# Optimization experiments

Measured on AMD Instinct MI355X. Metric: run time of the kernel, lower is better.

Reference implementation:

```python
import jax, jax.numpy as jnp
import numpy as np

H = 16  # num_heads
LN_EPS = 1e-5


def setup_inputs() -> dict:
    key = jax.random.key(0)
    ks = jax.random.split(key, 9)
    B, T, D = 2, 2048, 1024
    s = D ** -0.5
    return {
        "q": jax.random.normal(ks[0], (B, T, D), jnp.float32),
        "k": jax.random.normal(ks[1], (B, T, D), jnp.float32),
        "v": jax.random.normal(ks[2], (B, T, D), jnp.float32),
        "wq": jax.random.normal(ks[3], (D, D), jnp.float32) * s,
        "bq": jnp.zeros((D,), jnp.float32),
        "wk": jax.random.normal(ks[4], (D, D), jnp.float32) * s,
        "bk": jnp.zeros((D,), jnp.float32),
        "wv": jax.random.normal(ks[5], (D, D), jnp.float32) * s,
        "bv": jnp.zeros((D,), jnp.float32),
        "ln_g": jnp.ones((D,), jnp.float32),
        "ln_b": jnp.zeros((D,), jnp.float32),
    }


def _layernorm(x, g, b):
    mu = jnp.mean(x, axis=-1, keepdims=True)
    var = jnp.mean(jnp.square(x - mu), axis=-1, keepdims=True)
    return (x - mu) * jax.lax.rsqrt(var + LN_EPS) * g + b


def reference(q, k, v, wq, bq, wk, bk, wv, bv, ln_g, ln_b):
    B, T, D = q.shape
    dh = D // H
    residual = q
    qp = q @ wq.T + bq
    kp = k @ wk.T + bk
    vp = v @ wv.T + bv
    # faithful to torch: flat row-major view (B,T,D) -> (H*B, T, dh)
    qh = qp.reshape(H * B, T, dh)
    kh = kp.reshape(H * B, T, dh)
    vh = vp.reshape(H * B, T, dh)
    scores = jnp.einsum('btd,bsd->bts', qh, kh) * (dh ** -0.5)  # (H*B, T, T)
    attn = jax.nn.softmax(scores, axis=-1)
    ctx = jnp.einsum('bts,bsd->btd', attn, vh)  # (H*B, T, dh)
    ctx = ctx.reshape(B, T, D)
    out = _layernorm(residual + ctx, ln_g, ln_b)
    return (out, attn)
```

## Files before the change

kernel.cpp:

```cpp
#include <hip/hip_runtime.h>

typedef unsigned short u16;
typedef __attribute__((ext_vector_type(8))) short s8v;
typedef __attribute__((ext_vector_type(4))) float f4v;

#define MFMA16(a, b, c) __builtin_amdgcn_mfma_f32_16x16x32_bf16(a, b, c, 0, 0, 0)

#define TSEQ 2048
#define NTOK 4096
#define HEADS 32
#define HB_ELEMS 131072

__device__ __forceinline__ unsigned cvt_pk(float lo, float hi) {
  unsigned r;
  asm("v_cvt_pk_bf16_f32 %0, %1, %2" : "=v"(r) : "v"(lo), "v"(hi));
  return r;
}

__device__ __forceinline__ void gl_lds16(const u16* g, u16* l) {
  __builtin_amdgcn_global_load_lds(
      (const __attribute__((address_space(1))) void*)g,
      (__attribute__((address_space(3))) void*)l, 16, 0, 0);
}

__global__ void cvt_all(const float* __restrict__ q, const float* __restrict__ k,
                        const float* __restrict__ v, const float* __restrict__ wq,
                        const float* __restrict__ wk, const float* __restrict__ wv,
                        u16* __restrict__ dst) {
  int i = (blockIdx.x * blockDim.x + threadIdx.x) * 4;
  const float* src; int off;
  if (i < 12582912) {
    int s = i >> 22; src = (s == 0) ? q : ((s == 1) ? k : v); off = i & 4194303;
  } else {
    int j = i - 12582912;
    int s = j >> 20; src = (s == 0) ? wq : ((s == 1) ? wk : wv); off = j & 1048575;
  }
  float4 val = *(const float4*)(src + off);
  uint2 o;
  o.x = cvt_pk(val.x, val.y);
  o.y = cvt_pk(val.z, val.w);
  *(uint2*)(dst + i) = o;
}

__launch_bounds__(256, 3)
__global__ void proj_gemm(const u16* __restrict__ Aall, const u16* __restrict__ Wall,
                          const float* __restrict__ bqp, const float* __restrict__ bkp,
                          const float* __restrict__ bvp, u16* __restrict__ Call) {
  const int z = blockIdx.z;
  const u16* A = Aall + (size_t)z * 4194304;
  const u16* W = Wall + (size_t)z * 1048576;
  u16* C = Call + (size_t)z * 4194304;
  const float* bias = (z == 0) ? bqp : ((z == 1) ? bkp : bvp);

  __shared__ __align__(16) u16 SH[17408];
  u16* As = SH;
  u16* Bs = SH + 8192;

  const int tid = threadIdx.x;
  const int w = tid >> 6, lane = tid & 63, g = lane >> 4, l = lane & 15;
  const int wr = w >> 1, wc = w & 1;
  const int tr = blockIdx.y * 128, tc = blockIdx.x * 128;

  const int srow = tid >> 3;
  const int scol = (tid & 7) * 8;

  f4v acc[4][4] = {};

  for (int kt = 0; kt < 1024; kt += 64) {
#pragma unroll
    for (int c4 = 0; c4 < 4; ++c4) {
      gl_lds16(A + (size_t)(tr + c4 * 32 + srow) * 1024 + kt + scol,
               As + c4 * 2048 + tid * 8);
      gl_lds16(W + (size_t)(tc + c4 * 32 + srow) * 1024 + kt + scol,
               Bs + c4 * 2048 + tid * 8);
    }
    __syncthreads();
#pragma unroll
    for (int ks = 0; ks < 2; ++ks) {
      s8v a[4], bb[4];
#pragma unroll
      for (int m = 0; m < 4; ++m)
        a[m] = *(const s8v*)(As + (wr * 64 + m * 16 + l) * 64 + ks * 32 + g * 8);
#pragma unroll
      for (int n = 0; n < 4; ++n)
        bb[n] = *(const s8v*)(Bs + (wc * 64 + n * 16 + l) * 64 + ks * 32 + g * 8);
#pragma unroll
      for (int m = 0; m < 4; ++m)
#pragma unroll
        for (int n = 0; n < 4; ++n)
          acc[m][n] = MFMA16(a[m], bb[n], acc[m][n]);
    }
    __syncthreads();
  }
  u16* T = SH;
#pragma unroll
  for (int m = 0; m < 4; ++m)
#pragma unroll
    for (int n = 0; n < 4; ++n) {
      int d = wc * 64 + n * 16 + l;
      float bv = bias[tc + d];
      unsigned c01 = cvt_pk(acc[m][n][0] + bv, acc[m][n][1] + bv);
      unsigned c23 = cvt_pk(acc[m][n][2] + bv, acc[m][n][3] + bv);
      int t0 = wr * 64 + m * 16 + g * 4;
      T[(t0 + 0) * 136 + d] = (u16)c01;
      T[(t0 + 1) * 136 + d] = (u16)(c01 >> 16);
      T[(t0 + 2) * 136 + d] = (u16)c23;
      T[(t0 + 3) * 136 + d] = (u16)(c23 >> 16);
    }
  __syncthreads();
#pragma unroll
  for (int it = 0; it < 8; ++it) {
    int t = it * 16 + (tid >> 4);
    int c8 = (tid & 15) * 8;
    *(s8v*)(C + (size_t)(tr + t) * 1024 + tc + c8) = *(const s8v*)&T[t * 136 + c8];
  }
}

__global__ void vtrans(const u16* __restrict__ vp, u16* __restrict__ vT) {
  const int hb = blockIdx.y;
  const int t0 = blockIdx.x * 64;
  const int tid = threadIdx.x;
  __shared__ u16 tl[64][65];
  const u16* vph = vp + (size_t)hb * HB_ELEMS;
  u16* vth = vT + (size_t)hb * HB_ELEMS;
#pragma unroll
  for (int it = 0; it < 4; ++it) {
    int i = (tid + it * 256) * 4;
    int r = i >> 6, c = i & 63;
    *(ushort4*)&tl[r][c] = *(const ushort4*)(vph + (size_t)(t0 + r) * 64 + c);
  }
  __syncthreads();
#pragma unroll
  for (int it = 0; it < 4; ++it) {
    int i = (tid + it * 256) * 4;
    int d = i >> 6, j = i & 63;
    ushort4 o;
    o.x = tl[j + 0][d]; o.y = tl[j + 1][d]; o.z = tl[j + 2][d]; o.w = tl[j + 3][d];
    *(ushort4*)(vth + (size_t)d * TSEQ + t0 + j) = o;
  }
}

__launch_bounds__(512, 2)
__global__ void attn_fused(const u16* __restrict__ qp, const u16* __restrict__ kp,
                           const u16* __restrict__ vT, float* __restrict__ attn,
                           float* __restrict__ ctx) {
  const int hw = blockIdx.x + (blockIdx.y << 4);
  const int hb = (hw & 7) + ((hw >> 7) << 3);
  const int qt = (hw >> 3) & 15;

  const int tid = threadIdx.x;
  const int w = tid >> 6, lane = tid & 63, g = lane >> 4, l = lane & 15;
  const int lx = l & 7;

  const u16* qh = qp + (size_t)hb * HB_ELEMS;
  const u16* kh = kp + (size_t)hb * HB_ELEMS;
  const u16* vh = vT + (size_t)hb * HB_ELEMS;

  __shared__ __align__(16) u16 SH[35840];

  const int row0 = qt * 128 + w * 16;
  const float scale = 0.125f;

  const int srow = tid >> 3;
  const int swc = ((tid & 7) ^ (srow & 7)) * 8;

  s8v qf0 = *(const s8v*)(qh + (size_t)(row0 + l) * 64 + g * 8);
  s8v qf1 = *(const s8v*)(qh + (size_t)(row0 + l) * 64 + 32 + g * 8);

#define STAGE1(buf, kt4_) do { const int c0_ = (kt4_) * 256;                    \
    _Pragma("unroll")                                                           \
    for (int c4 = 0; c4 < 4; ++c4)                                              \
      gl_lds16(kh + (size_t)(c0_ + c4 * 64 + srow) * 64 + swc,                  \
               (buf) + c4 * 4096 + tid * 8);                                    \
  } while (0)

  u16* Ka = SH;
  u16* Kb = SH + 16384;

  float sum = 0.0f;
  STAGE1(Ka, 0);
  asm volatile("s_waitcnt vmcnt(0)" ::: "memory");
  __builtin_amdgcn_sched_barrier(0);
  __builtin_amdgcn_s_barrier();
  for (int kt4 = 0; kt4 < 8; ++kt4) {
    const u16* kbuf = (kt4 & 1) ? Kb : Ka;
    if (kt4 < 7) STAGE1((kt4 & 1) ? Ka : Kb, kt4 + 1);
#pragma unroll
    for (int q4 = 0; q4 < 4; ++q4) {
#pragma unroll
      for (int n = 0; n < 4; ++n) {
        const u16* kr = kbuf + q4 * 4096 + (n * 16 + l) * 64;
        s8v b0 = *(const s8v*)(kr + (g ^ lx) * 8);
        s8v b1 = *(const s8v*)(kr + ((4 + g) ^ lx) * 8);
        f4v s = {};
        s = MFMA16(b0, qf0, s);
        s = MFMA16(b1, qf1, s);
        sum += __expf(s[0] * scale) + __expf(s[1] * scale)
             + __expf(s[2] * scale) + __expf(s[3] * scale);
      }
    }
    asm volatile("s_waitcnt lgkmcnt(0)" ::: "memory");
    asm volatile("s_waitcnt vmcnt(0)" ::: "memory");
    __builtin_amdgcn_sched_barrier(0);
    __builtin_amdgcn_s_barrier();
  }
#undef STAGE1
  sum += __shfl_xor(sum, 16);
  sum += __shfl_xor(sum, 32);
  const float inv = 1.0f / sum;

  u16* K0 = SH;
  u16* V0 = SH + 8192;
  float* Pf = (float*)(SH + 16384);

#define STAGE2(b, kt_) do { const int c0_ = (kt_) * 64;                          \
    gl_lds16(kh + (size_t)(c0_ + srow) * 64 + swc, K0 + (b) * 4096 + tid * 8);   \
    gl_lds16(vh + (size_t)srow * TSEQ + c0_ + swc, V0 + (b) * 4096 + tid * 8);   \
  } while (0)

  f4v cacc[4] = {};
  float* attn_h = attn + (size_t)hb * TSEQ * TSEQ;
  const int kt0 = (qt * 2 + ((hw >> 7) << 3)) & 31;
  const int prow = w * 16 + l;
  const int sr4 = lane >> 4;
  const int sc = (lane & 15) * 4;

  STAGE2(0, kt0);
  asm volatile("s_waitcnt vmcnt(0)" ::: "memory");
  __builtin_amdgcn_sched_barrier(0);
  __builtin_amdgcn_s_barrier();

  for (int i = 0; i < 32; ++i) {
    const int cur = i & 1;
    const int col0 = ((i + kt0) & 31) * 64;
    const u16* Kl = K0 + cur * 4096;
    const u16* Vl = V0 + cur * 4096;
    if (i < 31) STAGE2(cur ^ 1, (i + 1 + kt0) & 31);
#pragma unroll
    for (int n = 0; n < 4; ++n) {
      const u16* kr = Kl + (n * 16 + l) * 64;
      s8v b0 = *(const s8v*)(kr + (g ^ lx) * 8);
      s8v b1 = *(const s8v*)(kr + ((4 + g) ^ lx) * 8);
      f4v s = {};
      s = MFMA16(b0, qf0, s);
      s = MFMA16(b1, qf1, s);
      f4v p;
#pragma unroll
      for (int r = 0; r < 4; ++r) p[r] = __expf(s[r] * scale) * inv;
      *(f4v*)&Pf[prow * 76 + n * 16 + g * 4] = p;
    }
    asm volatile("s_waitcnt lgkmcnt(0)" ::: "memory");
    __builtin_amdgcn_sched_barrier(0);
#pragma unroll
    for (int ks = 0; ks < 2; ++ks) {
      const float* pr = &Pf[prow * 76 + ks * 32 + g * 8];
      f4v r0 = *(const f4v*)pr;
      f4v r1 = *(const f4v*)(pr + 4);
      union { unsigned u[4]; s8v s; } pc;
      pc.u[0] = cvt_pk(r0[0], r0[1]);
      pc.u[1] = cvt_pk(r0[2], r0[3]);
      pc.u[2] = cvt_pk(r1[0], r1[1]);
      pc.u[3] = cvt_pk(r1[2], r1[3]);
      s8v pa = pc.s;
#pragma unroll
      for (int n4 = 0; n4 < 4; ++n4) {
        const u16* vr = Vl + (n4 * 16 + l) * 64;
        s8v bvv = *(const s8v*)(vr + ((ks * 4 + g) ^ lx) * 8);
        cacc[n4] = MFMA16(pa, bvv, cacc[n4]);
      }
    }
#pragma unroll
    for (int r4 = 0; r4 < 4; ++r4) {
      const int row = w * 16 + r4 * 4 + sr4;
      f4v pv_ = *(const f4v*)&Pf[row * 76 + sc];
      *(f4v*)(attn_h + (size_t)(qt * 128 + row) * TSEQ + col0 + sc) = pv_;
    }
    if (i < 31) {
      asm volatile("s_waitcnt lgkmcnt(0)" ::: "memory");
      asm volatile("s_waitcnt vmcnt(4)" ::: "memory");
      __builtin_amdgcn_sched_barrier(0);
      __builtin_amdgcn_s_barrier();
    }
  }
#undef STAGE2
#pragma unroll
  for (int n4 = 0; n4 < 4; ++n4)
#pragma unroll
    for (int r = 0; r < 4; ++r)
      ctx[(size_t)hb * HB_ELEMS + (size_t)(row0 + g * 4 + r) * 64 + n4 * 16 + l] =
          cacc[n4][r];
}

__global__ void ln_kernel(const float* __restrict__ q, const float* __restrict__ ctx,
                          const float* __restrict__ gam, const float* __restrict__ bet,
                          float* __restrict__ out) {
  const int row = blockIdx.x;
  const int tid = threadIdx.x;
  const float* qr = q + (size_t)row * 1024;
  const float* cr = ctx + (size_t)row * 1024;
  float4 xq = *(const float4*)(qr + tid * 4);
  float4 xc = *(const float4*)(cr + tid * 4);
  float x0 = xq.x + xc.x, x1 = xq.y + xc.y, x2 = xq.z + xc.z, x3 = xq.w + xc.w;
  float s1 = x0 + x1 + x2 + x3;
  float s2 = x0 * x0 + x1 * x1 + x2 * x2 + x3 * x3;
#pragma unroll
  for (int off = 1; off < 64; off <<= 1) {
    s1 += __shfl_xor(s1, off);
    s2 += __shfl_xor(s2, off);
  }
  __shared__ float ra[4], rb[4];
  int w = tid >> 6, lane = tid & 63;
  if (lane == 0) { ra[w] = s1; rb[w] = s2; }
  __syncthreads();
  s1 = ra[0] + ra[1] + ra[2] + ra[3];
  s2 = rb[0] + rb[1] + rb[2] + rb[3];
  float mu = s1 * (1.0f / 1024.0f);
  float var = s2 * (1.0f / 1024.0f) - mu * mu;
  float rstd = rsqrtf(var + 1e-5f);
  float4 gv = *(const float4*)(gam + tid * 4);
  float4 bv = *(const float4*)(bet + tid * 4);
  float4 o;
  o.x = (x0 - mu) * rstd * gv.x + bv.x;
  o.y = (x1 - mu) * rstd * gv.y + bv.y;
  o.z = (x2 - mu) * rstd * gv.z + bv.z;
  o.w = (x3 - mu) * rstd * gv.w + bv.w;
  *(float4*)(out + (size_t)row * 1024 + tid * 4) = o;
}

extern "C" void kernel_launch(void* const* d_in, const int* in_sizes, int n_in,
                              void* d_out, int out_size, void* d_ws, size_t ws_size,
                              hipStream_t stream) {
  const float* q    = (const float*)d_in[0];
  const float* k    = (const float*)d_in[1];
  const float* v    = (const float*)d_in[2];
  const float* wq   = (const float*)d_in[3];
  const float* bq   = (const float*)d_in[4];
  const float* wk   = (const float*)d_in[5];
  const float* bk   = (const float*)d_in[6];
  const float* wv   = (const float*)d_in[7];
  const float* bv   = (const float*)d_in[8];
  const float* ln_g = (const float*)d_in[9];
  const float* ln_b = (const float*)d_in[10];

  char* ws = (char*)d_ws;
  u16* qbf  = (u16*)(ws);
  u16* wbf  = (u16*)(ws + 25165824);
  u16* qp   = (u16*)(ws + 31457280);
  u16* vT   = (u16*)(ws + 56623104);
  float* ctx = (float*)(ws + 65011712);

  float* out  = (float*)d_out;
  float* attn = out + 4194304;

  cvt_all<<<15360, 256, 0, stream>>>(q, k, v, wq, wk, wv, qbf);

  proj_gemm<<<dim3(8, 32, 3), 256, 0, stream>>>(qbf, wbf, bq, bk, bv, qp);

  vtrans<<<dim3(32, 32), 256, 0, stream>>>(qp + 8388608, vT);

  attn_fused<<<dim3(16, 32), 512, 0, stream>>>(qp, qp + 4194304, vT, attn, ctx);

  ln_kernel<<<4096, 256, 0, stream>>>(q, ctx, ln_g, ln_b, out);
}
```

Baseline: 210.1 us.

## Double-buffer projection GEMM LDS tiles with XOR-swizzled layout

The projection GEMM mainloop now uses two LDS buffers with a K-step of 32. The next tile is issued through global_load_lds while MFMAs run on the current one, so the load latency that used to sit behind __syncthreads is meant to be hidden. The LDS tile layout is XOR-swizzled on 8-element column groups to cut bank conflicts on the MFMA fragment reads. In exchange there are twice as many barrier iterations, each with only 16 MFMAs, and explicit waitcnt plus sched barriers that may limit how much overlap the compiler can produce.

```diff
diff --git a/kernel.cpp b/kernel.cpp
--- a/kernel.cpp
+++ b/kernel.cpp
@@ -53,45 +53,59 @@
   const float* bias = (z == 0) ? bqp : ((z == 1) ? bkp : bvp);
 
   __shared__ __align__(16) u16 SH[17408];
-  u16* As = SH;
-  u16* Bs = SH + 8192;
 
   const int tid = threadIdx.x;
   const int w = tid >> 6, lane = tid & 63, g = lane >> 4, l = lane & 15;
   const int wr = w >> 1, wc = w & 1;
   const int tr = blockIdx.y * 128, tc = blockIdx.x * 128;
 
-  const int srow = tid >> 3;
-  const int scol = (tid & 7) * 8;
+  const int srow = tid >> 2;
+  const int swc = ((tid & 3) ^ (srow & 3)) * 8;
+  const int lx3 = l & 3;
+
+#define PSTAGE(buf, kt_) do {                                                   \
+    _Pragma("unroll")                                                           \
+    for (int c2 = 0; c2 < 2; ++c2) {                                            \
+      gl_lds16(A + (size_t)(tr + c2 * 64 + srow) * 1024 + (kt_) + swc,          \
+               (buf) + c2 * 2048 + tid * 8);                                    \
+      gl_lds16(W + (size_t)(tc + c2 * 64 + srow) * 1024 + (kt_) + swc,          \
+               (buf) + 4096 + c2 * 2048 + tid * 8);                             \
+    }                                                                           \
+  } while (0)
 
   f4v acc[4][4] = {};
 
-  for (int kt = 0; kt < 1024; kt += 64) {
-#pragma unroll
-    for (int c4 = 0; c4 < 4; ++c4) {
-      gl_lds16(A + (size_t)(tr + c4 * 32 + srow) * 1024 + kt + scol,
-               As + c4 * 2048 + tid * 8);
-      gl_lds16(W + (size_t)(tc + c4 * 32 + srow) * 1024 + kt + scol,
-               Bs + c4 * 2048 + tid * 8);
-    }
-    __syncthreads();
-#pragma unroll
-    for (int ks = 0; ks < 2; ++ks) {
-      s8v a[4], bb[4];
-#pragma unroll
-      for (int m = 0; m < 4; ++m)
-        a[m] = *(const s8v*)(As + (wr * 64 + m * 16 + l) * 64 + ks * 32 + g * 8);
+  PSTAGE(SH, 0);
+  asm volatile("s_waitcnt vmcnt(0)" ::: "memory");
+  __builtin_amdgcn_sched_barrier(0);
+  __builtin_amdgcn_s_barrier();
+
+  for (int i = 0; i < 32; ++i) {
+    u16* buf = SH + (i & 1) * 8192;
+    if (i < 31) PSTAGE(SH + ((i + 1) & 1) * 8192, (i + 1) * 32);
+    s8v a[4], bb[4];
+#pragma unroll
+    for (int m = 0; m < 4; ++m) {
+      const int R = wr * 64 + m * 16 + l;
+      a[m] = *(const s8v*)(buf + R * 32 + ((g ^ lx3) * 8));
+    }
+#pragma unroll
+    for (int n = 0; n < 4; ++n) {
+      const int R = wc * 64 + n * 16 + l;
+      bb[n] = *(const s8v*)(buf + 4096 + R * 32 + ((g ^ lx3) * 8));
+    }
+#pragma unroll
+    for (int m = 0; m < 4; ++m)
 #pragma unroll
       for (int n = 0; n < 4; ++n)
-        bb[n] = *(const s8v*)(Bs + (wc * 64 + n * 16 + l) * 64 + ks * 32 + g * 8);
-#pragma unroll
-      for (int m = 0; m < 4; ++m)
-#pragma unroll
-        for (int n = 0; n < 4; ++n)
-          acc[m][n] = MFMA16(a[m], bb[n], acc[m][n]);
-    }
-    __syncthreads();
-  }
+        acc[m][n] = MFMA16(a[m], bb[n], acc[m][n]);
+    asm volatile("s_waitcnt lgkmcnt(0)" ::: "memory");
+    asm volatile("s_waitcnt vmcnt(0)" ::: "memory");
+    __builtin_amdgcn_sched_barrier(0);
+    __builtin_amdgcn_s_barrier();
+  }
+#undef PSTAGE
+
   u16* T = SH;
 #pragma unroll
   for (int m = 0; m < 4; ++m)
```

Result: no change. 209.8 us (-0.1%).
